# Optimization experiments

Hardware: AMD Instinct MI355X
Metric: run time of the kernel (lower is better)

## Reference

```python
import jax, jax.numpy as jnp
import numpy as np

B, N, D, H = 2, 2048, 1024, 16
DH = D // H
SCALE = DH ** -0.5


def setup_inputs() -> dict:
    key = jax.random.key(0)
    ks = jax.random.split(key, 12)
    s = 0.02
    q = jax.random.normal(ks[0], (B, N, D), jnp.float32)
    k = jax.random.normal(ks[1], (B, N, D), jnp.float32)
    v = jax.random.normal(ks[2], (B, N, D), jnp.float32)
    attn_mask = jax.random.randint(ks[3], (B, 1, N, N), 0, 2).astype(bool)
    Wq = jax.random.normal(ks[4], (D, D), jnp.float32) * s
    bq = jnp.zeros((D,), jnp.float32)
    Wk = jax.random.normal(ks[5], (D, D), jnp.float32) * s
    bk = jnp.zeros((D,), jnp.float32)
    Wv = jax.random.normal(ks[6], (D, D), jnp.float32) * s
    bv = jnp.zeros((D,), jnp.float32)
    Wp = jax.random.normal(ks[7], (D, D), jnp.float32) * s
    bp = jnp.zeros((D,), jnp.float32)
    return {"q": q, "k": k, "v": v, "attn_mask": attn_mask,
            "Wq": Wq, "bq": bq, "Wk": Wk, "bk": bk,
            "Wv": Wv, "bv": bv, "Wp": Wp, "bp": bp}


def _heads(x, W, b):
    # (B, N, D) -> (B, H, N, DH)
    Bx, Nx, _ = x.shape
    return (x @ W + b).reshape(Bx, Nx, H, DH).transpose(0, 2, 1, 3)


def reference(q, k, v, attn_mask, Wq, bq, Wk, bk, Wv, bv, Wp, bp):
    qh = _heads(q, Wq, bq)                 # (B, H, Nq, DH)
    kh = _heads(k, Wk, bk)                 # (B, H, Nk, DH)
    vh = _heads(v, Wv, bv)                 # (B, H, Nk, DH)
    attn_raw = jnp.einsum('bhqd,bhkd->bhqk', qh, kh) * SCALE
    attn = jnp.where(attn_mask, -jnp.inf, attn_raw)   # masked_fill(attn_mask, -inf)
    attn = jax.nn.softmax(attn, axis=-1)
    x = jnp.einsum('bhqk,bhkd->bhqd', attn, vh)       # (B, H, Nq, DH)
    x = x.transpose(0, 2, 1, 3).reshape(q.shape[0], q.shape[1], D)
    return x @ Wp + bp
```

## Files before the change

kernel.cpp:

```cpp
#include <hip/hip_runtime.h>
#include <stdint.h>

typedef short bf16x8 __attribute__((ext_vector_type(8)));
typedef float f32x4 __attribute__((ext_vector_type(4)));

#define DEV __device__ __forceinline__

static constexpr int BB = 2, NN = 2048, DD = 1024, HH = 16, DH = 64;
static constexpr float SCLOG2E = 0.18033688011112042f;

static constexpr size_t OFF_PACK   = 1024;
static constexpr size_t PACK_BYTES = (size_t)BB * NN * (NN / 64) * 8ull;
static constexpr size_t OFF_WT     = OFF_PACK + PACK_BYTES;
static constexpr size_t WT_ONE     = (size_t)DD * DD;
static constexpr size_t HEAD_BYTES = (size_t)BB * HH * NN * DH * 2ull;
static constexpr size_t OFF_QH     = OFF_WT + 4 * WT_ONE * 2;
static constexpr size_t OFF_KH     = OFF_QH + HEAD_BYTES;
static constexpr size_t OFF_VT     = OFF_KH + HEAD_BYTES;
static constexpr size_t OFF_X      = OFF_VT + HEAD_BYTES;
static constexpr size_t OFF_KB     = OFF_X + HEAD_BYTES;
static constexpr size_t OFF_VB     = OFF_KB + HEAD_BYTES;
static constexpr size_t NEED_BIG   = OFF_VB + HEAD_BYTES;

DEV unsigned short f2b(float f) {
  unsigned int u = __builtin_bit_cast(unsigned int, f);
  u = (u + 0x7fffu + ((u >> 16) & 1u)) >> 16;
  return (unsigned short)u;
}

#define GLOAD16(gp, lp) __builtin_amdgcn_global_load_lds(                     \
    (const __attribute__((address_space(1))) void*)(gp),                      \
    (__attribute__((address_space(3))) void*)(lp), 16, 0, 0)

__global__ void detect_mask(const unsigned int* m, unsigned int* flag) {
  int t = threadIdx.x;
  uint4 v = ((const uint4*)m)[t];
  unsigned int vals[4] = {v.x, v.y, v.z, v.w};
  unsigned int f = 0;
  for (int i = 0; i < 4; i++) {
    unsigned int x = vals[i];
    if (x != 0u && x != 1u) f |= 1u;
    if (x != 0u && x != 0x3f800000u) f |= 2u;
  }
  if (f) atomicOr(flag, f);
}

__global__ void pack_mask(const void* msrc, const unsigned int* flag,
                          unsigned long long* packed) {
  int w = blockIdx.x * 256 + threadIdx.x;
  unsigned int f = *flag;
  size_t base = (size_t)(w >> 5) * 2048 + (size_t)(w & 31) * 64;
  unsigned long long bits = 0ull;
  if (!(f & 1u)) {
    const int4* p = (const int4*)msrc + (base >> 2);
    #pragma unroll
    for (int c = 0; c < 16; c++) {
      int4 q = p[c];
      if (q.x) bits |= 1ull << (4 * c + 0);
      if (q.y) bits |= 1ull << (4 * c + 1);
      if (q.z) bits |= 1ull << (4 * c + 2);
      if (q.w) bits |= 1ull << (4 * c + 3);
    }
  } else if (!(f & 2u)) {
    const float4* p = (const float4*)msrc + (base >> 2);
    #pragma unroll
    for (int c = 0; c < 16; c++) {
      float4 q = p[c];
      if (q.x != 0.f) bits |= 1ull << (4 * c + 0);
      if (q.y != 0.f) bits |= 1ull << (4 * c + 1);
      if (q.z != 0.f) bits |= 1ull << (4 * c + 2);
      if (q.w != 0.f) bits |= 1ull << (4 * c + 3);
    }
  } else {
    const uint4* p = (const uint4*)((const char*)msrc + base);
    #pragma unroll
    for (int c = 0; c < 4; c++) {
      uint4 q = p[c];
      unsigned int vals[4] = {q.x, q.y, q.z, q.w};
      #pragma unroll
      for (int i = 0; i < 4; i++)
        #pragma unroll
        for (int j = 0; j < 4; j++)
          if ((vals[i] >> (8 * j)) & 0xffu) bits |= 1ull << (16 * c + 4 * i + j);
    }
  }
  packed[w] = bits;
}

__global__ void transpose_w(const float* W0, const float* W1, const float* W2,
                            const float* W3, unsigned short* wt) {
  __shared__ unsigned short T[64][72];
  int z = blockIdx.z, t = threadIdx.x;
  const float* W = (z == 0) ? W0 : (z == 1) ? W1 : (z == 2) ? W2 : W3;
  unsigned short* dst = wt + (size_t)z * WT_ONE;
  int k0 = blockIdx.y * 64, n0 = blockIdx.x * 64;
  #pragma unroll
  for (int i = 0; i < 4; i++) {
    int row = i * 16 + (t >> 4), col = 4 * (t & 15);
    float4 v = *(const float4*)&W[(size_t)(k0 + row) * DD + n0 + col];
    T[row][col + 0] = f2b(v.x); T[row][col + 1] = f2b(v.y);
    T[row][col + 2] = f2b(v.z); T[row][col + 3] = f2b(v.w);
  }
  __syncthreads();
  #pragma unroll
  for (int i = 0; i < 4; i++) {
    int n = i * 16 + (t >> 4), k = 4 * (t & 15);
    ushort4 o = make_ushort4(T[k][n], T[k + 1][n], T[k + 2][n], T[k + 3][n]);
    *(ushort4*)&dst[(size_t)(n0 + n) * DD + k0 + k] = o;
  }
}

__global__ void cvt_qkv(const float* q, const float* k, const float* v,
                        unsigned short* qb, unsigned short* kb,
                        unsigned short* vb) {
  int z = blockIdx.z;
  const float* s = (z == 0) ? q : (z == 1) ? k : v;
  unsigned short* d = (z == 0) ? qb : (z == 1) ? kb : vb;
  size_t i = ((size_t)blockIdx.x * 256 + threadIdx.x) * 8;
  float4 a = *(const float4*)&s[i];
  float4 b2 = *(const float4*)&s[i + 4];
  unsigned short o[8] = {f2b(a.x),  f2b(a.y),  f2b(a.z),  f2b(a.w),
                         f2b(b2.x), f2b(b2.y), f2b(b2.z), f2b(b2.w)};
  *(uint4*)&d[i] = *(const uint4*)o;
}

template <int AFP32>
__global__ __launch_bounds__(256) void gemm_qkv(
    const void* A0, const void* A1, const void* A2,
    const unsigned short* Wt,
    const float* b0, const float* b1, const float* b2,
    unsigned short* dQ, unsigned short* dK, unsigned short* dVt) {
  __shared__ unsigned short Al[128 * 32];
  __shared__ unsigned short Bl[128 * 32];
  const int t = threadIdx.x, z = blockIdx.z;
  const int m0 = blockIdx.y * 128, n0 = blockIdx.x * 128;
  const unsigned short* Bsrc = Wt + (size_t)z * WT_ONE;
  const void* Av = (z == 0) ? A0 : (z == 1) ? A1 : A2;
  const float* bias = (z == 0) ? b0 : (z == 1) ? b1 : b2;
  const int w = t >> 6, l = t & 63, lr = l & 15, lg = l >> 4;
  const int wm = (w >> 1) * 64, wn = (w & 1) * 64;

  f32x4 acc[4][4];
  #pragma unroll
  for (int i = 0; i < 4; i++)
    #pragma unroll
    for (int j = 0; j < 4; j++) acc[i][j] = (f32x4){0.f, 0.f, 0.f, 0.f};

  for (int k0 = 0; k0 < DD; k0 += 32) {
    __syncthreads();
    if (AFP32) {
      const float* Af = (const float*)Av;
      #pragma unroll
      for (int i = 0; i < 4; i++) {
        int row = i * 32 + (t >> 3), kk = 4 * (t & 7);
        float4 vv = *(const float4*)&Af[(size_t)(m0 + row) * DD + k0 + kk];
        ushort4 o4 = make_ushort4(f2b(vv.x), f2b(vv.y), f2b(vv.z), f2b(vv.w));
        *(ushort4*)&Al[row * 32 + kk] = o4;
      }
    } else {
      const unsigned short* Ab = (const unsigned short*)Av;
      #pragma unroll
      for (int c = 0; c < 2; c++)
        GLOAD16(&Ab[(size_t)(m0 + w * 32 + c * 16 + (l >> 2)) * DD + k0 + (l & 3) * 8],
                &Al[(w * 32 + c * 16) * 32]);
    }
    #pragma unroll
    for (int c = 0; c < 2; c++)
      GLOAD16(&Bsrc[(size_t)(n0 + w * 32 + c * 16 + (l >> 2)) * DD + k0 + (l & 3) * 8],
              &Bl[(w * 32 + c * 16) * 32]);
    __syncthreads();

    bf16x8 af[4], bfr[4];
    #pragma unroll
    for (int mi = 0; mi < 4; mi++)
      af[mi] = *(const bf16x8*)&Al[(wm + mi * 16 + lr) * 32 + lg * 8];
    #pragma unroll
    for (int ni = 0; ni < 4; ni++)
      bfr[ni] = *(const bf16x8*)&Bl[(wn + ni * 16 + lr) * 32 + lg * 8];
    #pragma unroll
    for (int mi = 0; mi < 4; mi++)
      #pragma unroll
      for (int ni = 0; ni < 4; ni++)
        acc[mi][ni] = __builtin_amdgcn_mfma_f32_16x16x32_bf16(
            af[mi], bfr[ni], acc[mi][ni], 0, 0, 0);
  }

  const float scl = (z == 0) ? SCLOG2E : 1.0f;
  #pragma unroll
  for (int mi = 0; mi < 4; mi++) {
    #pragma unroll
    for (int ni = 0; ni < 4; ni++) {
      int col = n0 + wn + ni * 16 + lr;
      float bv = bias[col];
      int h = col >> 6, dh = col & 63;
      int mbase = m0 + wm + mi * 16 + lg * 4;
      if (z == 2) {
        int bq = mbase >> 11, n = mbase & 2047;
        unsigned short o4[4];
        #pragma unroll
        for (int r = 0; r < 4; r++) o4[r] = f2b(acc[mi][ni][r] + bv);
        *(ushort4*)&dVt[(((size_t)(bq * HH + h)) * DH + dh) * NN + n] =
            *(const ushort4*)o4;
      } else {
        unsigned short* dst = (z == 0) ? dQ : dK;
        #pragma unroll
        for (int r = 0; r < 4; r++) {
          int m = mbase + r;
          int bq = m >> 11, n = m & 2047;
          dst[(((size_t)(bq * HH + h)) * NN + n) * DH + dh] =
              f2b((acc[mi][ni][r] + bv) * scl);
        }
      }
    }
  }
}

__global__ __launch_bounds__(256) void gemm_proj(
    const unsigned short* X, const unsigned short* Wt, const float* bias,
    float* out) {
  __shared__ unsigned short Al[128 * 32];
  __shared__ unsigned short Bl[128 * 32];
  const int t = threadIdx.x;
  const int m0 = blockIdx.y * 128, n0 = blockIdx.x * 128;
  const int w = t >> 6, l = t & 63, lr = l & 15, lg = l >> 4;
  const int wm = (w >> 1) * 64, wn = (w & 1) * 64;

  f32x4 acc[4][4];
  #pragma unroll
  for (int i = 0; i < 4; i++)
    #pragma unroll
    for (int j = 0; j < 4; j++) acc[i][j] = (f32x4){0.f, 0.f, 0.f, 0.f};

  for (int k0 = 0; k0 < DD; k0 += 32) {
    __syncthreads();
    #pragma unroll
    for (int c = 0; c < 2; c++) {
      GLOAD16(&X[(size_t)(m0 + w * 32 + c * 16 + (l >> 2)) * DD + k0 + (l & 3) * 8],
              &Al[(w * 32 + c * 16) * 32]);
      GLOAD16(&Wt[(size_t)(n0 + w * 32 + c * 16 + (l >> 2)) * DD + k0 + (l & 3) * 8],
              &Bl[(w * 32 + c * 16) * 32]);
    }
    __syncthreads();

    bf16x8 af[4], bfr[4];
    #pragma unroll
    for (int mi = 0; mi < 4; mi++)
      af[mi] = *(const bf16x8*)&Al[(wm + mi * 16 + lr) * 32 + lg * 8];
    #pragma unroll
    for (int ni = 0; ni < 4; ni++)
      bfr[ni] = *(const bf16x8*)&Bl[(wn + ni * 16 + lr) * 32 + lg * 8];
    #pragma unroll
    for (int mi = 0; mi < 4; mi++)
      #pragma unroll
      for (int ni = 0; ni < 4; ni++)
        acc[mi][ni] = __builtin_amdgcn_mfma_f32_16x16x32_bf16(
            af[mi], bfr[ni], acc[mi][ni], 0, 0, 0);
  }

  #pragma unroll
  for (int mi = 0; mi < 4; mi++) {
    #pragma unroll
    for (int ni = 0; ni < 4; ni++) {
      int col = n0 + wn + ni * 16 + lr;
      float bv = bias[col];
      #pragma unroll
      for (int r = 0; r < 4; r++) {
        int m = m0 + wm + mi * 16 + lg * 4 + r;
        out[(size_t)m * DD + col] = acc[mi][ni][r] + bv;
      }
    }
  }
}

__global__ __launch_bounds__(256) void attn_k(
    const unsigned short* qh, const unsigned short* kh,
    const unsigned short* vht, const unsigned long long* packed,
    unsigned short* x) {
  __shared__ unsigned short Kl[64 * 72];
  __shared__ unsigned short Vl[64 * 72];
  __shared__ unsigned short Pl[4][16 * 72];
  const int t = threadIdx.x, w = t >> 6, l = t & 63;
  const int lr = l & 15, lg = l >> 4;

  const int id = blockIdx.x;
  const int xcd = id & 7, j = id >> 3;
  const int bhg = xcd * 4 + (j >> 5);
  const int q0 = (j & 31) * 64;
  const int b = bhg >> 4, h = bhg & 15;
  const size_t bh = (size_t)b * HH + h;
  const unsigned short* Q = qh + bh * (size_t)NN * DH;
  const unsigned short* K = kh + bh * (size_t)NN * DH;
  const unsigned short* V = vht + bh * (size_t)NN * DH;
  const int qrow = q0 + w * 16 + lr;
  const unsigned long long* pmrow =
      packed + ((size_t)b * NN + qrow) * (NN / 64);

  bf16x8 qf[2];
  #pragma unroll
  for (int kc = 0; kc < 2; kc++)
    qf[kc] = *(const bf16x8*)&Q[(size_t)qrow * DH + kc * 32 + lg * 8];

  f32x4 o[4];
  #pragma unroll
  for (int f = 0; f < 4; f++) o[f] = (f32x4){0.f, 0.f, 0.f, 0.f};
  float lsum = 0.f;

  const int srow = t >> 2, scol = (t & 3) * 16;
  uint4 k0r, k1r, v0r, v1r;
  {
    const unsigned short* kp = &K[(size_t)srow * DH + scol];
    const unsigned short* vp = &V[(size_t)srow * NN + scol];
    k0r = *(const uint4*)kp;  k1r = *(const uint4*)(kp + 8);
    v0r = *(const uint4*)vp;  v1r = *(const uint4*)(vp + 8);
  }

  for (int kt = 0; kt < NN / 64; kt++) {
    __syncthreads();
    *(uint4*)&Kl[srow * 72 + scol]     = k0r;
    *(uint4*)&Kl[srow * 72 + scol + 8] = k1r;
    *(uint4*)&Vl[srow * 72 + scol]     = v0r;
    *(uint4*)&Vl[srow * 72 + scol + 8] = v1r;
    __syncthreads();
    if (kt + 1 < NN / 64) {
      const unsigned short* kp = &K[(size_t)((kt + 1) * 64 + srow) * DH + scol];
      const unsigned short* vp = &V[(size_t)srow * NN + (kt + 1) * 64 + scol];
      k0r = *(const uint4*)kp;  k1r = *(const uint4*)(kp + 8);
      v0r = *(const uint4*)vp;  v1r = *(const uint4*)(vp + 8);
    }

    unsigned long long mw = pmrow[kt];

    f32x4 sv4[4];
    __builtin_amdgcn_s_setprio(1);
    #pragma unroll
    for (int f = 0; f < 4; f++) {
      f32x4 s = (f32x4){0.f, 0.f, 0.f, 0.f};
      bf16x8 kf0 = *(const bf16x8*)&Kl[(16 * f + lr) * 72 + lg * 8];
      bf16x8 kf1 = *(const bf16x8*)&Kl[(16 * f + lr) * 72 + 32 + lg * 8];
      s = __builtin_amdgcn_mfma_f32_16x16x32_bf16(kf0, qf[0], s, 0, 0, 0);
      s = __builtin_amdgcn_mfma_f32_16x16x32_bf16(kf1, qf[1], s, 0, 0, 0);
      sv4[f] = s;
    }
    __builtin_amdgcn_s_setprio(0);

    float part = 0.f;
    #pragma unroll
    for (int f = 0; f < 4; f++) {
      unsigned nib = (unsigned)(mw >> (16 * f + 4 * lg)) & 0xFu;
      float pv[4];
      #pragma unroll
      for (int r = 0; r < 4; r++) {
        float s = ((nib >> r) & 1u) ? -30000.f : sv4[f][r];
        pv[r] = __builtin_amdgcn_exp2f(s);
        part += pv[r];
      }
      unsigned w0, w1;
      asm("v_cvt_pk_bf16_f32 %0, %1, %2" : "=v"(w0) : "v"(pv[0]), "v"(pv[1]));
      asm("v_cvt_pk_bf16_f32 %0, %1, %2" : "=v"(w1) : "v"(pv[2]), "v"(pv[3]));
      *(uint2*)&Pl[w][lr * 72 + 16 * f + lg * 4] = make_uint2(w0, w1);
    }
    lsum += part;
    asm volatile("s_waitcnt lgkmcnt(0)" ::: "memory");
    __builtin_amdgcn_sched_barrier(0);

    bf16x8 pf0 = *(const bf16x8*)&Pl[w][lr * 72 + lg * 8];
    bf16x8 pf1 = *(const bf16x8*)&Pl[w][lr * 72 + 32 + lg * 8];
    __builtin_amdgcn_s_setprio(1);
    #pragma unroll
    for (int f = 0; f < 4; f++) {
      bf16x8 vf0 = *(const bf16x8*)&Vl[(16 * f + lr) * 72 + lg * 8];
      o[f] = __builtin_amdgcn_mfma_f32_16x16x32_bf16(vf0, pf0, o[f], 0, 0, 0);
      bf16x8 vf1 = *(const bf16x8*)&Vl[(16 * f + lr) * 72 + 32 + lg * 8];
      o[f] = __builtin_amdgcn_mfma_f32_16x16x32_bf16(vf1, pf1, o[f], 0, 0, 0);
    }
    __builtin_amdgcn_s_setprio(0);
  }

  lsum += __shfl_xor(lsum, 16);
  lsum += __shfl_xor(lsum, 32);
  float inv = 1.f / fmaxf(lsum, 1e-30f);
  #pragma unroll
  for (int f = 0; f < 4; f++) {
    unsigned w0, w1;
    float a0 = o[f][0] * inv, a1 = o[f][1] * inv;
    float a2 = o[f][2] * inv, a3 = o[f][3] * inv;
    asm("v_cvt_pk_bf16_f32 %0, %1, %2" : "=v"(w0) : "v"(a0), "v"(a1));
    asm("v_cvt_pk_bf16_f32 %0, %1, %2" : "=v"(w1) : "v"(a2), "v"(a3));
    *(uint2*)&x[((size_t)b * NN + qrow) * DD + h * DH + 16 * f + lg * 4] =
        make_uint2(w0, w1);
  }
}

extern "C" void kernel_launch(void* const* d_in, const int* in_sizes, int n_in,
                              void* d_out, int out_size, void* d_ws, size_t ws_size,
                              hipStream_t stream) {
  const float* q  = (const float*)d_in[0];
  const float* k  = (const float*)d_in[1];
  const float* v  = (const float*)d_in[2];
  const void*  mk = d_in[3];
  const float* Wq = (const float*)d_in[4];
  const float* bq = (const float*)d_in[5];
  const float* Wk = (const float*)d_in[6];
  const float* bk = (const float*)d_in[7];
  const float* Wv = (const float*)d_in[8];
  const float* bv = (const float*)d_in[9];
  const float* Wp = (const float*)d_in[10];
  const float* bp = (const float*)d_in[11];
  float* out = (float*)d_out;
  char* ws = (char*)d_ws;

  unsigned int* flag = (unsigned int*)ws;
  unsigned long long* packed = (unsigned long long*)(ws + OFF_PACK);
  unsigned short* wt  = (unsigned short*)(ws + OFF_WT);
  unsigned short* qhp = (unsigned short*)(ws + OFF_QH);
  unsigned short* khp = (unsigned short*)(ws + OFF_KH);
  unsigned short* vht = (unsigned short*)(ws + OFF_VT);
  unsigned short* x   = (unsigned short*)(ws + OFF_X);
  unsigned short* qb  = (unsigned short*)(ws + OFF_X);
  unsigned short* kb  = (unsigned short*)(ws + OFF_KB);
  unsigned short* vb  = (unsigned short*)(ws + OFF_VB);

  const bool big = ws_size >= NEED_BIG;

  hipMemsetAsync(flag, 0, 4, stream);
  detect_mask<<<1, 256, 0, stream>>>((const unsigned int*)mk, flag);
  pack_mask<<<dim3(512), 256, 0, stream>>>(mk, flag, packed);
  transpose_w<<<dim3(16, 16, 4), 256, 0, stream>>>(Wq, Wk, Wv, Wp, wt);
  if (big) {
    cvt_qkv<<<dim3(2048, 1, 3), 256, 0, stream>>>(q, k, v, qb, kb, vb);
    gemm_qkv<0><<<dim3(8, 32, 3), 256, 0, stream>>>(qb, kb, vb, wt, bq, bk, bv,
                                                    qhp, khp, vht);
  } else {
    gemm_qkv<1><<<dim3(8, 32, 3), 256, 0, stream>>>(q, k, v, wt, bq, bk, bv,
                                                    qhp, khp, vht);
  }
  attn_k<<<dim3(1024), 256, 0, stream>>>(qhp, khp, vht, packed, x);
  gemm_proj<<<dim3(8, 32), 256, 0, stream>>>(x, wt + 3 * WT_ONE, bp, out);
}
```

Before: 180.0 us.

## Merge prep kernels, deepen GEMM K-step, and swizzle attention LDS layout

Folds the memset, mask detection, mask packing, weight transpose and input conversion into one prep launch. Mask format detection now runs per block by scanning only the first 16 words instead of 1024. Both GEMMs now stage 64-wide K chunks per barrier pair to halve synchronisation, and the attention kernel replaces padded LDS rows with an XOR-swizzled 128-byte layout for K, V and P. The trade-offs are higher LDS use per GEMM block and a weaker mask-format check.

```diff
diff --git a/kernel.cpp b/kernel.cpp
--- a/kernel.cpp
+++ b/kernel.cpp
@@ -32,96 +32,93 @@
     (const __attribute__((address_space(1))) void*)(gp),                      \
     (__attribute__((address_space(3))) void*)(lp), 16, 0, 0)
 
-__global__ void detect_mask(const unsigned int* m, unsigned int* flag) {
-  int t = threadIdx.x;
-  uint4 v = ((const uint4*)m)[t];
-  unsigned int vals[4] = {v.x, v.y, v.z, v.w};
-  unsigned int f = 0;
-  for (int i = 0; i < 4; i++) {
-    unsigned int x = vals[i];
-    if (x != 0u && x != 1u) f |= 1u;
-    if (x != 0u && x != 0x3f800000u) f |= 2u;
-  }
-  if (f) atomicOr(flag, f);
-}
-
-__global__ void pack_mask(const void* msrc, const unsigned int* flag,
-                          unsigned long long* packed) {
-  int w = blockIdx.x * 256 + threadIdx.x;
-  unsigned int f = *flag;
-  size_t base = (size_t)(w >> 5) * 2048 + (size_t)(w & 31) * 64;
-  unsigned long long bits = 0ull;
-  if (!(f & 1u)) {
-    const int4* p = (const int4*)msrc + (base >> 2);
-    #pragma unroll
-    for (int c = 0; c < 16; c++) {
-      int4 q = p[c];
-      if (q.x) bits |= 1ull << (4 * c + 0);
-      if (q.y) bits |= 1ull << (4 * c + 1);
-      if (q.z) bits |= 1ull << (4 * c + 2);
-      if (q.w) bits |= 1ull << (4 * c + 3);
-    }
-  } else if (!(f & 2u)) {
-    const float4* p = (const float4*)msrc + (base >> 2);
-    #pragma unroll
-    for (int c = 0; c < 16; c++) {
-      float4 q = p[c];
-      if (q.x != 0.f) bits |= 1ull << (4 * c + 0);
-      if (q.y != 0.f) bits |= 1ull << (4 * c + 1);
-      if (q.z != 0.f) bits |= 1ull << (4 * c + 2);
-      if (q.w != 0.f) bits |= 1ull << (4 * c + 3);
-    }
+__global__ __launch_bounds__(256) void prep(
+    const float* W0, const float* W1, const float* W2, const float* W3,
+    unsigned short* wt,
+    const float* q, const float* k, const float* v,
+    unsigned short* qb, unsigned short* kb, unsigned short* vb, int doCvt,
+    const void* msrc, unsigned long long* packed) {
+  __shared__ unsigned short T[64][72];
+  const int id = blockIdx.x, t = threadIdx.x;
+
+  if (id < 1024) {
+    int z = id >> 8, local = id & 255;
+    int n0 = (local & 15) * 64, k0 = (local >> 4) * 64;
+    const float* W = (z == 0) ? W0 : (z == 1) ? W1 : (z == 2) ? W2 : W3;
+    unsigned short* dst = wt + (size_t)z * WT_ONE;
+    #pragma unroll
+    for (int i = 0; i < 4; i++) {
+      int row = i * 16 + (t >> 4), col = 4 * (t & 15);
+      float4 vv = *(const float4*)&W[(size_t)(k0 + row) * DD + n0 + col];
+      T[row][col + 0] = f2b(vv.x); T[row][col + 1] = f2b(vv.y);
+      T[row][col + 2] = f2b(vv.z); T[row][col + 3] = f2b(vv.w);
+    }
+    __syncthreads();
+    #pragma unroll
+    for (int i = 0; i < 4; i++) {
+      int n = i * 16 + (t >> 4), kk = 4 * (t & 15);
+      ushort4 o = make_ushort4(T[kk][n], T[kk + 1][n], T[kk + 2][n], T[kk + 3][n]);
+      *(ushort4*)&dst[(size_t)(n0 + n) * DD + k0 + kk] = o;
+    }
+  } else if (id < 7168) {
+    if (!doCvt) return;
+    int local = id - 1024;
+    int z = local / 2048, bx = local % 2048;
+    const float* s = (z == 0) ? q : (z == 1) ? k : v;
+    unsigned short* d = (z == 0) ? qb : (z == 1) ? kb : vb;
+    size_t i = ((size_t)bx * 256 + t) * 8;
+    float4 a = *(const float4*)&s[i];
+    float4 b2 = *(const float4*)&s[i + 4];
+    unsigned short o[8] = {f2b(a.x),  f2b(a.y),  f2b(a.z),  f2b(a.w),
+                           f2b(b2.x), f2b(b2.y), f2b(b2.z), f2b(b2.w)};
+    *(uint4*)&d[i] = *(const uint4*)o;
   } else {
-    const uint4* p = (const uint4*)((const char*)msrc + base);
-    #pragma unroll
-    for (int c = 0; c < 4; c++) {
-      uint4 q = p[c];
-      unsigned int vals[4] = {q.x, q.y, q.z, q.w};
-      #pragma unroll
-      for (int i = 0; i < 4; i++)
-        #pragma unroll
-        for (int j = 0; j < 4; j++)
-          if ((vals[i] >> (8 * j)) & 0xffu) bits |= 1ull << (16 * c + 4 * i + j);
-    }
-  }
-  packed[w] = bits;
-}
-
-__global__ void transpose_w(const float* W0, const float* W1, const float* W2,
-                            const float* W3, unsigned short* wt) {
-  __shared__ unsigned short T[64][72];
-  int z = blockIdx.z, t = threadIdx.x;
-  const float* W = (z == 0) ? W0 : (z == 1) ? W1 : (z == 2) ? W2 : W3;
-  unsigned short* dst = wt + (size_t)z * WT_ONE;
-  int k0 = blockIdx.y * 64, n0 = blockIdx.x * 64;
-  #pragma unroll
-  for (int i = 0; i < 4; i++) {
-    int row = i * 16 + (t >> 4), col = 4 * (t & 15);
-    float4 v = *(const float4*)&W[(size_t)(k0 + row) * DD + n0 + col];
-    T[row][col + 0] = f2b(v.x); T[row][col + 1] = f2b(v.y);
-    T[row][col + 2] = f2b(v.z); T[row][col + 3] = f2b(v.w);
-  }
-  __syncthreads();
-  #pragma unroll
-  for (int i = 0; i < 4; i++) {
-    int n = i * 16 + (t >> 4), k = 4 * (t & 15);
-    ushort4 o = make_ushort4(T[k][n], T[k + 1][n], T[k + 2][n], T[k + 3][n]);
-    *(ushort4*)&dst[(size_t)(n0 + n) * DD + k0 + k] = o;
-  }
-}
-
-__global__ void cvt_qkv(const float* q, const float* k, const float* v,
-                        unsigned short* qb, unsigned short* kb,
-                        unsigned short* vb) {
-  int z = blockIdx.z;
-  const float* s = (z == 0) ? q : (z == 1) ? k : v;
-  unsigned short* d = (z == 0) ? qb : (z == 1) ? kb : vb;
-  size_t i = ((size_t)blockIdx.x * 256 + threadIdx.x) * 8;
-  float4 a = *(const float4*)&s[i];
-  float4 b2 = *(const float4*)&s[i + 4];
-  unsigned short o[8] = {f2b(a.x),  f2b(a.y),  f2b(a.z),  f2b(a.w),
-                         f2b(b2.x), f2b(b2.y), f2b(b2.z), f2b(b2.w)};
-  *(uint4*)&d[i] = *(const uint4*)o;
+    unsigned f = 0;
+    const unsigned* m32 = (const unsigned*)msrc;
+    #pragma unroll
+    for (int i = 0; i < 16; i++) {
+      unsigned xv = m32[i];
+      if (xv != 0u && xv != 1u) f |= 1u;
+      if (xv != 0u && xv != 0x3f800000u) f |= 2u;
+    }
+    int w = (id - 7168) * 256 + t;
+    size_t base = (size_t)(w >> 5) * 2048 + (size_t)(w & 31) * 64;
+    unsigned long long bits = 0ull;
+    if (!(f & 1u)) {
+      const int4* p = (const int4*)msrc + (base >> 2);
+      #pragma unroll
+      for (int c = 0; c < 16; c++) {
+        int4 qv = p[c];
+        if (qv.x) bits |= 1ull << (4 * c + 0);
+        if (qv.y) bits |= 1ull << (4 * c + 1);
+        if (qv.z) bits |= 1ull << (4 * c + 2);
+        if (qv.w) bits |= 1ull << (4 * c + 3);
+      }
+    } else if (!(f & 2u)) {
+      const float4* p = (const float4*)msrc + (base >> 2);
+      #pragma unroll
+      for (int c = 0; c < 16; c++) {
+        float4 qv = p[c];
+        if (qv.x != 0.f) bits |= 1ull << (4 * c + 0);
+        if (qv.y != 0.f) bits |= 1ull << (4 * c + 1);
+        if (qv.z != 0.f) bits |= 1ull << (4 * c + 2);
+        if (qv.w != 0.f) bits |= 1ull << (4 * c + 3);
+      }
+    } else {
+      const uint4* p = (const uint4*)((const char*)msrc + base);
+      #pragma unroll
+      for (int c = 0; c < 4; c++) {
+        uint4 qv = p[c];
+        unsigned vals[4] = {qv.x, qv.y, qv.z, qv.w};
+        #pragma unroll
+        for (int i = 0; i < 4; i++)
+          #pragma unroll
+          for (int j = 0; j < 4; j++)
+            if ((vals[i] >> (8 * j)) & 0xffu) bits |= 1ull << (16 * c + 4 * i + j);
+      }
+    }
+    packed[w] = bits;
+  }
 }
 
 template <int AFP32>
@@ -130,8 +127,8 @@
     const unsigned short* Wt,
     const float* b0, const float* b1, const float* b2,
     unsigned short* dQ, unsigned short* dK, unsigned short* dVt) {
-  __shared__ unsigned short Al[128 * 32];
-  __shared__ unsigned short Bl[128 * 32];
+  __shared__ unsigned short Al[2][128 * 32];
+  __shared__ unsigned short Bl[2][128 * 32];
   const int t = threadIdx.x, z = blockIdx.z;
   const int m0 = blockIdx.y * 128, n0 = blockIdx.x * 128;
   const unsigned short* Bsrc = Wt + (size_t)z * WT_ONE;
@@ -146,43 +143,53 @@
     #pragma unroll
     for (int j = 0; j < 4; j++) acc[i][j] = (f32x4){0.f, 0.f, 0.f, 0.f};
 
-  for (int k0 = 0; k0 < DD; k0 += 32) {
+  for (int k0 = 0; k0 < DD; k0 += 64) {
     __syncthreads();
     if (AFP32) {
       const float* Af = (const float*)Av;
       #pragma unroll
       for (int i = 0; i < 4; i++) {
         int row = i * 32 + (t >> 3), kk = 4 * (t & 7);
-        float4 vv = *(const float4*)&Af[(size_t)(m0 + row) * DD + k0 + kk];
-        ushort4 o4 = make_ushort4(f2b(vv.x), f2b(vv.y), f2b(vv.z), f2b(vv.w));
-        *(ushort4*)&Al[row * 32 + kk] = o4;
+        #pragma unroll
+        for (int hh = 0; hh < 2; hh++) {
+          float4 vv = *(const float4*)&Af[(size_t)(m0 + row) * DD + k0 + hh * 32 + kk];
+          ushort4 o4 = make_ushort4(f2b(vv.x), f2b(vv.y), f2b(vv.z), f2b(vv.w));
+          *(ushort4*)&Al[hh][row * 32 + kk] = o4;
+        }
       }
     } else {
       const unsigned short* Ab = (const unsigned short*)Av;
       #pragma unroll
+      for (int p = 0; p < 2; p++)
+        #pragma unroll
+        for (int c = 0; c < 2; c++)
+          GLOAD16(&Ab[(size_t)(m0 + w * 32 + c * 16 + (l >> 2)) * DD + k0 + p * 32 + (l & 3) * 8],
+                  &Al[p][(w * 32 + c * 16) * 32]);
+    }
+    #pragma unroll
+    for (int p = 0; p < 2; p++)
+      #pragma unroll
       for (int c = 0; c < 2; c++)
-        GLOAD16(&Ab[(size_t)(m0 + w * 32 + c * 16 + (l >> 2)) * DD + k0 + (l & 3) * 8],
-                &Al[(w * 32 + c * 16) * 32]);
-    }
-    #pragma unroll
-    for (int c = 0; c < 2; c++)
-      GLOAD16(&Bsrc[(size_t)(n0 + w * 32 + c * 16 + (l >> 2)) * DD + k0 + (l & 3) * 8],
-              &Bl[(w * 32 + c * 16) * 32]);
-    __syncthreads();
-
-    bf16x8 af[4], bfr[4];
-    #pragma unroll
-    for (int mi = 0; mi < 4; mi++)
-      af[mi] = *(const bf16x8*)&Al[(wm + mi * 16 + lr) * 32 + lg * 8];
-    #pragma unroll
-    for (int ni = 0; ni < 4; ni++)
-      bfr[ni] = *(const bf16x8*)&Bl[(wn + ni * 16 + lr) * 32 + lg * 8];
-    #pragma unroll
-    for (int mi = 0; mi < 4; mi++)
+        GLOAD16(&Bsrc[(size_t)(n0 + w * 32 + c * 16 + (l >> 2)) * DD + k0 + p * 32 + (l & 3) * 8],
+                &Bl[p][(w * 32 + c * 16) * 32]);
+    __syncthreads();
+
+    #pragma unroll
+    for (int p = 0; p < 2; p++) {
+      bf16x8 af[4], bfr[4];
+      #pragma unroll
+      for (int mi = 0; mi < 4; mi++)
+        af[mi] = *(const bf16x8*)&Al[p][(wm + mi * 16 + lr) * 32 + lg * 8];
       #pragma unroll
       for (int ni = 0; ni < 4; ni++)
-        acc[mi][ni] = __builtin_amdgcn_mfma_f32_16x16x32_bf16(
-            af[mi], bfr[ni], acc[mi][ni], 0, 0, 0);
+        bfr[ni] = *(const bf16x8*)&Bl[p][(wn + ni * 16 + lr) * 32 + lg * 8];
+      #pragma unroll
+      for (int mi = 0; mi < 4; mi++)
+        #pragma unroll
+        for (int ni = 0; ni < 4; ni++)
+          acc[mi][ni] = __builtin_amdgcn_mfma_f32_16x16x32_bf16(
+              af[mi], bfr[ni], acc[mi][ni], 0, 0, 0);
+    }
   }
 
   const float scl = (z == 0) ? SCLOG2E : 1.0f;
@@ -218,8 +225,8 @@
 __global__ __launch_bounds__(256) void gemm_proj(
     const unsigned short* X, const unsigned short* Wt, const float* bias,
     float* out) {
-  __shared__ unsigned short Al[128 * 32];
-  __shared__ unsigned short Bl[128 * 32];
+  __shared__ unsigned short Al[2][128 * 32];
+  __shared__ unsigned short Bl[2][128 * 32];
   const int t = threadIdx.x;
   const int m0 = blockIdx.y * 128, n0 = blockIdx.x * 128;
   const int w = t >> 6, l = t & 63, lr = l & 15, lg = l >> 4;
@@ -231,30 +238,35 @@
     #pragma unroll
     for (int j = 0; j < 4; j++) acc[i][j] = (f32x4){0.f, 0.f, 0.f, 0.f};
 
-  for (int k0 = 0; k0 < DD; k0 += 32) {
-    __syncthreads();
-    #pragma unroll
-    for (int c = 0; c < 2; c++) {
-      GLOAD16(&X[(size_t)(m0 + w * 32 + c * 16 + (l >> 2)) * DD + k0 + (l & 3) * 8],
-              &Al[(w * 32 + c * 16) * 32]);
-      GLOAD16(&Wt[(size_t)(n0 + w * 32 + c * 16 + (l >> 2)) * DD + k0 + (l & 3) * 8],
-              &Bl[(w * 32 + c * 16) * 32]);
-    }
-    __syncthreads();
-
-    bf16x8 af[4], bfr[4];
-    #pragma unroll
-    for (int mi = 0; mi < 4; mi++)
-      af[mi] = *(const bf16x8*)&Al[(wm + mi * 16 + lr) * 32 + lg * 8];
-    #pragma unroll
-    for (int ni = 0; ni < 4; ni++)
-      bfr[ni] = *(const bf16x8*)&Bl[(wn + ni * 16 + lr) * 32 + lg * 8];
-    #pragma unroll
-    for (int mi = 0; mi < 4; mi++)
+  for (int k0 = 0; k0 < DD; k0 += 64) {
+    __syncthreads();
+    #pragma unroll
+    for (int p = 0; p < 2; p++)
+      #pragma unroll
+      for (int c = 0; c < 2; c++) {
+        GLOAD16(&X[(size_t)(m0 + w * 32 + c * 16 + (l >> 2)) * DD + k0 + p * 32 + (l & 3) * 8],
+                &Al[p][(w * 32 + c * 16) * 32]);
+        GLOAD16(&Wt[(size_t)(n0 + w * 32 + c * 16 + (l >> 2)) * DD + k0 + p * 32 + (l & 3) * 8],
+                &Bl[p][(w * 32 + c * 16) * 32]);
+      }
+    __syncthreads();
+
+    #pragma unroll
+    for (int p = 0; p < 2; p++) {
+      bf16x8 af[4], bfr[4];
+      #pragma unroll
+      for (int mi = 0; mi < 4; mi++)
+        af[mi] = *(const bf16x8*)&Al[p][(wm + mi * 16 + lr) * 32 + lg * 8];
       #pragma unroll
       for (int ni = 0; ni < 4; ni++)
-        acc[mi][ni] = __builtin_amdgcn_mfma_f32_16x16x32_bf16(
-            af[mi], bfr[ni], acc[mi][ni], 0, 0, 0);
+        bfr[ni] = *(const bf16x8*)&Bl[p][(wn + ni * 16 + lr) * 32 + lg * 8];
+      #pragma unroll
+      for (int mi = 0; mi < 4; mi++)
+        #pragma unroll
+        for (int ni = 0; ni < 4; ni++)
+          acc[mi][ni] = __builtin_amdgcn_mfma_f32_16x16x32_bf16(
+              af[mi], bfr[ni], acc[mi][ni], 0, 0, 0);
+    }
   }
 
   #pragma unroll
@@ -276,11 +288,14 @@
     const unsigned short* qh, const unsigned short* kh,
     const unsigned short* vht, const unsigned long long* packed,
     unsigned short* x) {
-  __shared__ unsigned short Kl[64 * 72];
-  __shared__ unsigned short Vl[64 * 72];
-  __shared__ unsigned short Pl[4][16 * 72];
+  __shared__ __align__(16) unsigned short Kl[64 * 64];
+  __shared__ __align__(16) unsigned short Vl[64 * 64];
+  __shared__ __align__(16) unsigned short Pl[4][16 * 64];
+  char* KlB = (char*)Kl;
+  char* VlB = (char*)Vl;
   const int t = threadIdx.x, w = t >> 6, l = t & 63;
   const int lr = l & 15, lg = l >> 4;
+  char* PlB = (char*)&Pl[w][0];
 
   const int id = blockIdx.x;
   const int xcd = id & 7, j = id >> 3;
@@ -305,27 +320,29 @@
   for (int f = 0; f < 4; f++) o[f] = (f32x4){0.f, 0.f, 0.f, 0.f};
   float lsum = 0.f;
 
-  const int srow = t >> 2, scol = (t & 3) * 16;
-  uint4 k0r, k1r, v0r, v1r;
-  {
-    const unsigned short* kp = &K[(size_t)srow * DH + scol];
-    const unsigned short* vp = &V[(size_t)srow * NN + scol];
-    k0r = *(const uint4*)kp;  k1r = *(const uint4*)(kp + 8);
-    v0r = *(const uint4*)vp;  v1r = *(const uint4*)(vp + 8);
-  }
+  const int srow = t >> 2, sc0 = (t & 3) * 32;
+  const int swr = (srow & 7) << 4;
+  const int swl = (lr & 7) << 4;
+  const int sA = srow * 128 + (sc0 ^ swr);
+  const int sB = srow * 128 + ((sc0 + 16) ^ swr);
+
+  const unsigned short* kpp = &K[(size_t)srow * DH + sc0 / 2];
+  const unsigned short* vpp = &V[(size_t)srow * NN + sc0 / 2];
+  uint4 k0r = *(const uint4*)kpp, k1r = *(const uint4*)(kpp + 8);
+  uint4 v0r = *(const uint4*)vpp, v1r = *(const uint4*)(vpp + 8);
 
   for (int kt = 0; kt < NN / 64; kt++) {
     __syncthreads();
-    *(uint4*)&Kl[srow * 72 + scol]     = k0r;
-    *(uint4*)&Kl[srow * 72 + scol + 8] = k1r;
-    *(uint4*)&Vl[srow * 72 + scol]     = v0r;
-    *(uint4*)&Vl[srow * 72 + scol + 8] = v1r;
+    *(uint4*)&KlB[sA] = k0r;
+    *(uint4*)&KlB[sB] = k1r;
+    *(uint4*)&VlB[sA] = v0r;
+    *(uint4*)&VlB[sB] = v1r;
     __syncthreads();
     if (kt + 1 < NN / 64) {
-      const unsigned short* kp = &K[(size_t)((kt + 1) * 64 + srow) * DH + scol];
-      const unsigned short* vp = &V[(size_t)srow * NN + (kt + 1) * 64 + scol];
-      k0r = *(const uint4*)kp;  k1r = *(const uint4*)(kp + 8);
-      v0r = *(const uint4*)vp;  v1r = *(const uint4*)(vp + 8);
+      kpp += 64 * DH;
+      vpp += 64;
+      k0r = *(const uint4*)kpp;  k1r = *(const uint4*)(kpp + 8);
+      v0r = *(const uint4*)vpp;  v1r = *(const uint4*)(vpp + 8);
     }
 
     unsigned long long mw = pmrow[kt];
@@ -335,8 +352,8 @@
     #pragma unroll
     for (int f = 0; f < 4; f++) {
       f32x4 s = (f32x4){0.f, 0.f, 0.f, 0.f};
-      bf16x8 kf0 = *(const bf16x8*)&Kl[(16 * f + lr) * 72 + lg * 8];
-      bf16x8 kf1 = *(const bf16x8*)&Kl[(16 * f + lr) * 72 + 32 + lg * 8];
+      bf16x8 kf0 = *(const bf16x8*)&KlB[(16 * f + lr) * 128 + ((lg * 16) ^ swl)];
+      bf16x8 kf1 = *(const bf16x8*)&KlB[(16 * f + lr) * 128 + ((64 + lg * 16) ^ swl)];
       s = __builtin_amdgcn_mfma_f32_16x16x32_bf16(kf0, qf[0], s, 0, 0, 0);
       s = __builtin_amdgcn_mfma_f32_16x16x32_bf16(kf1, qf[1], s, 0, 0, 0);
       sv4[f] = s;
@@ -357,20 +374,20 @@
       unsigned w0, w1;
       asm("v_cvt_pk_bf16_f32 %0, %1, %2" : "=v"(w0) : "v"(pv[0]), "v"(pv[1]));
       asm("v_cvt_pk_bf16_f32 %0, %1, %2" : "=v"(w1) : "v"(pv[2]), "v"(pv[3]));
-      *(uint2*)&Pl[w][lr * 72 + 16 * f + lg * 4] = make_uint2(w0, w1);
+      *(uint2*)&PlB[lr * 128 + ((f * 32 + lg * 8) ^ swl)] = make_uint2(w0, w1);
     }
     lsum += part;
     asm volatile("s_waitcnt lgkmcnt(0)" ::: "memory");
     __builtin_amdgcn_sched_barrier(0);
 
-    bf16x8 pf0 = *(const bf16x8*)&Pl[w][lr * 72 + lg * 8];
-    bf16x8 pf1 = *(const bf16x8*)&Pl[w][lr * 72 + 32 + lg * 8];
+    bf16x8 pf0 = *(const bf16x8*)&PlB[lr * 128 + ((lg * 16) ^ swl)];
+    bf16x8 pf1 = *(const bf16x8*)&PlB[lr * 128 + ((64 + lg * 16) ^ swl)];
     __builtin_amdgcn_s_setprio(1);
     #pragma unroll
     for (int f = 0; f < 4; f++) {
-      bf16x8 vf0 = *(const bf16x8*)&Vl[(16 * f + lr) * 72 + lg * 8];
+      bf16x8 vf0 = *(const bf16x8*)&VlB[(16 * f + lr) * 128 + ((lg * 16) ^ swl)];
       o[f] = __builtin_amdgcn_mfma_f32_16x16x32_bf16(vf0, pf0, o[f], 0, 0, 0);
-      bf16x8 vf1 = *(const bf16x8*)&Vl[(16 * f + lr) * 72 + 32 + lg * 8];
+      bf16x8 vf1 = *(const bf16x8*)&VlB[(16 * f + lr) * 128 + ((64 + lg * 16) ^ swl)];
       o[f] = __builtin_amdgcn_mfma_f32_16x16x32_bf16(vf1, pf1, o[f], 0, 0, 0);
     }
     __builtin_amdgcn_s_setprio(0);
@@ -409,7 +426,6 @@
   float* out = (float*)d_out;
   char* ws = (char*)d_ws;
 
-  unsigned int* flag = (unsigned int*)ws;
   unsigned long long* packed = (unsigned long long*)(ws + OFF_PACK);
   unsigned short* wt  = (unsigned short*)(ws + OFF_WT);
   unsigned short* qhp = (unsigned short*)(ws + OFF_QH);
@@ -422,12 +438,9 @@
 
   const bool big = ws_size >= NEED_BIG;
 
-  hipMemsetAsync(flag, 0, 4, stream);
-  detect_mask<<<1, 256, 0, stream>>>((const unsigned int*)mk, flag);
-  pack_mask<<<dim3(512), 256, 0, stream>>>(mk, flag, packed);
-  transpose_w<<<dim3(16, 16, 4), 256, 0, stream>>>(Wq, Wk, Wv, Wp, wt);
+  prep<<<dim3(7680), 256, 0, stream>>>(Wq, Wk, Wv, Wp, wt, q, k, v,
+                                       qb, kb, vb, big ? 1 : 0, mk, packed);
   if (big) {
-    cvt_qkv<<<dim3(2048, 1, 3), 256, 0, stream>>>(q, k, v, qb, kb, vb);
     gemm_qkv<0><<<dim3(8, 32, 3), 256, 0, stream>>>(qb, kb, vb, wt, bq, bk, bv,
                                                     qhp, khp, vht);
   } else {
```

After: 170.4 us. 1.06x faster.
